# Optimization experiments

Hardware: AMD Instinct MI355X
Metric: run time of the kernel (lower is better)

## Reference

```python
import jax, jax.numpy as jnp
import numpy as np

H = 16
NEG = -1e10

def setup_inputs() -> dict:
    key = jax.random.key(0)
    ks = jax.random.split(key, 12)
    B, S, D = 2, 2048, 1024
    sc = 1.0 / np.sqrt(D)
    inp = {
        'q': jax.random.normal(ks[0], (B, S, D), jnp.float32),
        'k': jax.random.normal(ks[1], (B, S, D), jnp.float32),
        'v': jax.random.normal(ks[2], (B, S, D), jnp.float32),
        'Wq': jax.random.normal(ks[3], (D, D), jnp.float32) * sc,
        'bq': jax.random.normal(ks[4], (D,), jnp.float32) * 0.02,
        'Wk': jax.random.normal(ks[5], (D, D), jnp.float32) * sc,
        'bk': jax.random.normal(ks[6], (D,), jnp.float32) * 0.02,
        'Wv': jax.random.normal(ks[7], (D, D), jnp.float32) * sc,
        'bv': jax.random.normal(ks[8], (D,), jnp.float32) * 0.02,
        'Wo': jax.random.normal(ks[9], (D, D), jnp.float32) * sc,
        'bo': jax.random.normal(ks[10], (D,), jnp.float32) * 0.02,
        'mask': jax.random.randint(ks[11], (B, S, S), 0, 2, jnp.int32),
    }
    return inp

def reference(q, k, v, Wq, bq, Wk, bk, Wv, bv, Wo, bo, mask):
    B, S, D = q.shape
    dk = D // H
    # projections (torch Linear: x @ W.T + b), split heads -> [B,H,S,dk]
    qh = (q @ Wq.T + bq).reshape(B, S, H, dk).transpose(0, 2, 1, 3)
    kh = (k @ Wk.T + bk).reshape(B, S, H, dk).transpose(0, 2, 1, 3)
    vh = (v @ Wv.T + bv).reshape(B, S, H, dk).transpose(0, 2, 1, 3)
    # scaled dot-product scores [B,H,Sq,Sk]
    scores = jnp.einsum('bhqd,bhkd->bhqk', qh, kh) / jnp.sqrt(jnp.float32(dk))
    scores = jnp.where(mask[:, None, :, :] == 0, jnp.float32(NEG), scores)
    attn = jax.nn.softmax(scores, axis=-1)  # dropout in eval mode = identity
    ctx = jnp.einsum('bhqk,bhkd->bhqd', attn, vh)
    concat = ctx.transpose(0, 2, 1, 3).reshape(B, S, D)
    return concat @ Wo.T + bo
```

## Files before the change

### kernel.cpp

```cpp
#include <hip/hip_runtime.h>
#include <hip/hip_bf16.h>
#include <stdint.h>

typedef __bf16 bf16;
typedef __bf16 bf16x2 __attribute__((ext_vector_type(2)));
typedef __bf16 bf16x4 __attribute__((ext_vector_type(4)));
typedef __bf16 bf16x8 __attribute__((ext_vector_type(8)));
typedef float f32x4 __attribute__((ext_vector_type(4)));
typedef float f32x16 __attribute__((ext_vector_type(16)));
typedef unsigned int u32;
typedef u32 u32x4 __attribute__((ext_vector_type(4)));
typedef unsigned long long u64;

#define MFMA16(a, b, c) __builtin_amdgcn_mfma_f32_16x16x32_bf16((a), (b), (c), 0, 0, 0)
#define MFMA32(a, b, c) __builtin_amdgcn_mfma_f32_32x32x16_bf16((a), (b), (c), 0, 0, 0)

constexpr int Bc = 2, Sc = 2048, Dc = 1024, Hc = 16, DKc = 64;
constexpr int Mc = Bc * Sc;
constexpr int MW = Sc / 64;
#define QSCALE 0.1803368801111731f

__device__ __forceinline__ u32 pk2(float a, float b) {
  bf16x2 t; t[0] = (bf16)a; t[1] = (bf16)b;
  return __builtin_bit_cast(u32, t);
}

__device__ __forceinline__ void gl_lds16(const void* g, void* l) {
  __builtin_amdgcn_global_load_lds((const __attribute__((address_space(1))) void*)g,
                                   (__attribute__((address_space(3))) void*)l, 16, 0, 0);
}

__global__ __launch_bounds__(256) void convert_kernel(
    const float* __restrict__ wq, const float* __restrict__ wk,
    const float* __restrict__ wv, const float* __restrict__ wo,
    const float* __restrict__ q, const float* __restrict__ k, const float* __restrict__ v,
    bf16* __restrict__ dwq, bf16* __restrict__ dwk, bf16* __restrict__ dwv,
    bf16* __restrict__ dwo, bf16* __restrict__ dq, bf16* __restrict__ dk,
    bf16* __restrict__ dv) {
  const int y = blockIdx.y;
  const float* src; bf16* dst; size_t n;
  switch (y) {
    case 0: src = wq; dst = dwq; n = (size_t)Dc * Dc; break;
    case 1: src = wk; dst = dwk; n = (size_t)Dc * Dc; break;
    case 2: src = wv; dst = dwv; n = (size_t)Dc * Dc; break;
    case 3: src = wo; dst = dwo; n = (size_t)Dc * Dc; break;
    case 4: src = q;  dst = dq;  n = (size_t)Mc * Dc; break;
    case 5: src = k;  dst = dk;  n = (size_t)Mc * Dc; break;
    default: src = v; dst = dv;  n = (size_t)Mc * Dc; break;
  }
  const size_t i = ((size_t)blockIdx.x * 256 + threadIdx.x) * 8;
  if (i >= n) return;
  const float sc = (y == 0) ? QSCALE : 1.0f;
  f32x4 x0 = *(const f32x4*)&src[i];
  f32x4 x1 = *(const f32x4*)&src[i + 4];
  bf16x8 o;
#pragma unroll
  for (int j = 0; j < 4; ++j) { o[j] = (bf16)(x0[j] * sc); o[4 + j] = (bf16)(x1[j] * sc); }
  *(bf16x8*)&dst[i] = o;
}

__global__ __launch_bounds__(256) void packmask_kernel(const int* __restrict__ mask,
                                                       u64* __restrict__ mbT, int nwords) {
  const int lane = threadIdx.x & 63;
  const int wid = (blockIdx.x * blockDim.x + threadIdx.x) >> 6;
  const int nw = (gridDim.x * blockDim.x) >> 6;
  for (int i = wid; i < nwords; i += nw) {
    int v = mask[(size_t)i * 64 + lane];
    u64 bits = __ballot(v != 0);
    if (lane == 0) {
      const int kw = i & (MW - 1), bq = i >> 5;
      const int b = bq >> 11, q = bq & (Sc - 1);
      mbT[((size_t)(b * MW + kw)) * Sc + q] = bits;
    }
  }
}

__global__ __launch_bounds__(256, 3) void gemm_qkv_kernel(
    const bf16* __restrict__ qb, const bf16* __restrict__ kb, const bf16* __restrict__ vb,
    const bf16* __restrict__ wq, const bf16* __restrict__ wk, const bf16* __restrict__ wv,
    const float* __restrict__ bq, const float* __restrict__ bk, const float* __restrict__ bv,
    bf16* __restrict__ qh, bf16* __restrict__ kh, bf16* __restrict__ vt) {
  __shared__ bf16 As[128 * 64];
  __shared__ bf16 Bs[128 * 64];
  const int d = blockIdx.x;
  const int xcd = d & 7, idx = d >> 3;
  const int proj = idx >> 5, w = idx & 31;
  const int n0 = (w & 7) * 128;
  const int m0 = (xcd * 4 + (w >> 3)) * 128;
  const bf16* Af = proj == 0 ? qb : proj == 1 ? kb : vb;
  const bf16* Bw = proj == 0 ? wq : proj == 1 ? wk : wv;
  const float* bias = proj == 0 ? bq : proj == 1 ? bk : bv;

  const int t = threadIdx.x, lane = t & 63, wv4 = t >> 6;
  const int c = lane & 15, g = lane >> 4;
  const int wr = wv4 >> 1, wc = wv4 & 1;

  f32x4 acc[4][4];
#pragma unroll
  for (int i = 0; i < 4; ++i)
#pragma unroll
    for (int j = 0; j < 4; ++j) acc[i][j] = (f32x4){0.f, 0.f, 0.f, 0.f};

  const int brow_l = lane >> 3;
  const int bslot_l = (lane & 7) ^ brow_l;

  for (int k0 = 0; k0 < Dc; k0 += 64) {
#pragma unroll
    for (int u = 0; u < 4; ++u) {
      const int ch = wv4 * 4 + u;
      const int row = ch * 8 + brow_l;
      gl_lds16(&Af[(size_t)(m0 + row) * Dc + k0 + bslot_l * 8], &As[ch * 512]);
    }
#pragma unroll
    for (int u = 0; u < 4; ++u) {
      const int ch = wv4 * 4 + u;
      const int row = ch * 8 + brow_l;
      gl_lds16(&Bw[(size_t)(n0 + row) * Dc + k0 + bslot_l * 8], &Bs[ch * 512]);
    }
    __syncthreads();
#pragma unroll
    for (int ks = 0; ks < 2; ++ks) {
      bf16x8 af[4], bfr[4];
#pragma unroll
      for (int mt = 0; mt < 4; ++mt) {
        const int row = wr * 64 + mt * 16 + c;
        const int sl = (4 * ks + g) ^ (c & 7);
        af[mt] = *(const bf16x8*)&As[row * 64 + sl * 8];
      }
#pragma unroll
      for (int nt = 0; nt < 4; ++nt) {
        const int row = wc * 64 + nt * 16 + c;
        const int sl = (4 * ks + g) ^ (c & 7);
        bfr[nt] = *(const bf16x8*)&Bs[row * 64 + sl * 8];
      }
#pragma unroll
      for (int mt = 0; mt < 4; ++mt)
#pragma unroll
        for (int nt = 0; nt < 4; ++nt) acc[mt][nt] = MFMA16(af[mt], bfr[nt], acc[mt][nt]);
    }
    __syncthreads();
  }

  const float bsc = proj == 0 ? QSCALE : 1.0f;
  const int colb = n0 + wc * 64 + c;
  const int mrowb = m0 + wr * 64 + 4 * g;
#pragma unroll
  for (int mt = 0; mt < 4; ++mt) {
#pragma unroll
    for (int nt = 0; nt < 4; ++nt) {
      const int col = colb + nt * 16;
      const int mrow = mrowb + mt * 16;
      const float bb = bias[col] * bsc;
      f32x4 a = acc[mt][nt];
      if (proj == 0) {
#pragma unroll
        for (int r = 0; r < 4; ++r) qh[(size_t)(mrow + r) * Dc + col] = (bf16)(a[r] + bb);
      } else if (proj == 1) {
        const int hh = col >> 6, dd = col & 63;
#pragma unroll
        for (int r = 0; r < 4; ++r) {
          const int mr = mrow + r;
          kh[((size_t)((mr >> 11) * Hc + hh) * Sc + (mr & (Sc - 1))) * DKc + dd] = (bf16)(a[r] + bb);
        }
      } else {
        const int batch = mrow >> 11, s = mrow & (Sc - 1);
        const int s2 = (s & ~15) | ((s & 4) << 1) | ((s & 8) >> 1);
        const int hh = col >> 6, dd = col & 63;
        bf16x4 pkv;
#pragma unroll
        for (int r = 0; r < 4; ++r) pkv[r] = (bf16)(a[r] + bb);
        *(bf16x4*)&vt[((size_t)((batch * Hc + hh) * DKc + dd)) * Sc + s2] = pkv;
      }
    }
  }
}

__global__ __launch_bounds__(256, 2) void gemm_o_kernel(const bf16* __restrict__ ctxp,
                                                        const bf16* __restrict__ wo,
                                                        const float* __restrict__ bo,
                                                        float* __restrict__ outp) {
  __shared__ bf16 As[128 * 64];
  __shared__ bf16 Bs[64 * 64];
  const int d = blockIdx.x;
  const int xcd = d & 7, idx = d >> 3;
  const int n0 = (idx & 15) * 64;
  const int m0 = (xcd * 4 + (idx >> 4)) * 128;

  const int t = threadIdx.x, lane = t & 63, wv4 = t >> 6;
  const int c = lane & 15, g = lane >> 4;
  const int brow_l = lane >> 3;
  const int bslot_l = (lane & 7) ^ brow_l;

  f32x4 acc[2][4];
#pragma unroll
  for (int i = 0; i < 2; ++i)
#pragma unroll
    for (int j = 0; j < 4; ++j) acc[i][j] = (f32x4){0.f, 0.f, 0.f, 0.f};

  for (int k0 = 0; k0 < Dc; k0 += 64) {
#pragma unroll
    for (int u = 0; u < 4; ++u) {
      const int ch = wv4 * 4 + u;
      const int row = ch * 8 + brow_l;
      gl_lds16(&ctxp[(size_t)(m0 + row) * Dc + k0 + bslot_l * 8], &As[ch * 512]);
    }
    {
      const int ch = wv4;
      const int row = ch * 8 + brow_l;
      gl_lds16(&wo[(size_t)(n0 + row) * Dc + k0 + bslot_l * 8], &Bs[ch * 512]);
      const int ch2 = 4 + wv4;
      const int row2 = ch2 * 8 + brow_l;
      gl_lds16(&wo[(size_t)(n0 + row2) * Dc + k0 + bslot_l * 8], &Bs[ch2 * 512]);
    }
    __syncthreads();
#pragma unroll
    for (int ks = 0; ks < 2; ++ks) {
      bf16x8 af[2], bfr[4];
#pragma unroll
      for (int mt = 0; mt < 2; ++mt) {
        const int row = wv4 * 32 + mt * 16 + c;
        const int sl = (4 * ks + g) ^ (c & 7);
        af[mt] = *(const bf16x8*)&As[row * 64 + sl * 8];
      }
#pragma unroll
      for (int nt = 0; nt < 4; ++nt) {
        const int row = nt * 16 + c;
        const int sl = (4 * ks + g) ^ (c & 7);
        bfr[nt] = *(const bf16x8*)&Bs[row * 64 + sl * 8];
      }
#pragma unroll
      for (int mt = 0; mt < 2; ++mt)
#pragma unroll
        for (int nt = 0; nt < 4; ++nt) acc[mt][nt] = MFMA16(af[mt], bfr[nt], acc[mt][nt]);
    }
    __syncthreads();
  }

  const int colb = n0 + c;
  const int mrowb = m0 + wv4 * 32 + 4 * g;
#pragma unroll
  for (int mt = 0; mt < 2; ++mt)
#pragma unroll
    for (int nt = 0; nt < 4; ++nt) {
      const int col = colb + nt * 16;
      const int mrow = mrowb + mt * 16;
      const float bb = bo[col];
      f32x4 a = acc[mt][nt];
#pragma unroll
      for (int r = 0; r < 4; ++r) outp[(size_t)(mrow + r) * Dc + col] = a[r] + bb;
    }
}

template <int SPLITS>
__global__ __launch_bounds__(256, 4) void attn_kernel(const bf16* __restrict__ qh,
                                                      const bf16* __restrict__ kh,
                                                      const bf16* __restrict__ vt,
                                                      const u64* __restrict__ mbT,
                                                      bf16* __restrict__ ctx,
                                                      float* __restrict__ opart,
                                                      float2* __restrict__ ml) {
  __shared__ bf16 Ks[2][64 * 64];
  __shared__ bf16 Vs[2][64 * 64];
  const int d = blockIdx.x;
  const int xcd = d & 7, idx = d >> 3;
  int bh, qt, half;
  if constexpr (SPLITS == 2) {
    bh = xcd * 4 + (idx >> 5);
    const int sub = idx & 31;
    qt = sub >> 1; half = sub & 1;
  } else {
    bh = xcd * 4 + (idx >> 4);
    qt = idx & 15; half = 0;
  }
  const int b = bh >> 4, h = bh & 15;
  const int lane = threadIdx.x & 63, wv4 = threadIdx.x >> 6;
  const int ql = lane & 31, hi = lane >> 5;
  const int qrow = qt * 128 + wv4 * 32 + ql;

  const bf16* Qp = qh + (size_t)(b * Sc + qrow) * Dc + h * DKc;
  const bf16* Kp = kh + (size_t)(b * Hc + h) * Sc * DKc;
  const bf16* Vp = vt + (size_t)(b * Hc + h) * DKc * Sc;
  const u64* mbp = mbT + (size_t)b * MW * Sc;

  const int k0 = half * (Sc / SPLITS);
  constexpr int NIT = (Sc / SPLITS) / 64;

  const int srow = lane >> 3, sslot = lane & 7;
  auto stage = [&](int buf, int kt) {
#pragma unroll
    for (int u = 0; u < 2; ++u) {
      const int ch = wv4 * 2 + u;
      const int r = ch * 8 + srow;
      gl_lds16(&Kp[(size_t)(kt + r) * DKc + (size_t)((sslot ^ (r & 7)) * 8)], &Ks[buf][ch * 512]);
    }
#pragma unroll
    for (int u = 0; u < 2; ++u) {
      const int ch = wv4 * 2 + u;
      const int r = ch * 8 + srow;
      gl_lds16(&Vp[(size_t)r * Sc + kt + (size_t)((sslot ^ (r & 7)) * 8)], &Vs[buf][ch * 512]);
    }
  };

  bf16x8 qf[4];
#pragma unroll
  for (int ka = 0; ka < 4; ++ka) qf[ka] = *(const bf16x8*)&Qp[16 * ka + 8 * hi];

  bf16x8 ones8;
#pragma unroll
  for (int j = 0; j < 8; ++j) ones8[j] = (bf16)1.0f;

  f32x16 oacc[2], lacc;
#pragma unroll
  for (int i = 0; i < 2; ++i)
#pragma unroll
    for (int r = 0; r < 16; ++r) oacc[i][r] = 0.f;
#pragma unroll
  for (int r = 0; r < 16; ++r) lacc[r] = 0.f;

  stage(0, k0);
  u64 w = mbp[(size_t)(k0 >> 6) * Sc + qrow];
  asm volatile("s_waitcnt vmcnt(0)" ::: "memory");
  __builtin_amdgcn_s_barrier();
  __builtin_amdgcn_sched_barrier(0);

  for (int it = 0; it < NIT; ++it) {
    const int kt = k0 + it * 64;
    const int buf = it & 1;
    const int ktn = (it + 1 < NIT) ? kt + 64 : kt;
    stage(buf ^ 1, ktn);
    const u64 wn = mbp[(size_t)(ktn >> 6) * Sc + qrow];

    f32x16 st[2];
#pragma unroll
    for (int tt = 0; tt < 2; ++tt) {
      const int row = 32 * tt + ql;
      const bf16* kbase = &Ks[buf][row * 64];
      f32x16 z;
#pragma unroll
      for (int r = 0; r < 16; ++r) z[r] = 0.f;
      __builtin_amdgcn_s_setprio(1);
#pragma unroll
      for (int ka = 0; ka < 4; ++ka) {
        bf16x8 kf = *(const bf16x8*)&kbase[((2 * ka + hi) ^ (row & 7)) * 8];
        z = MFMA32(kf, qf[ka], z);
      }
      __builtin_amdgcn_s_setprio(0);
      st[tt] = z;
    }

    const u32 wt0 = (u32)(w >> (4 * hi));
    const u32 wt1 = (u32)(w >> (32 + 4 * hi));
#pragma unroll
    for (int tt = 0; tt < 2; ++tt) {
      const u32 wt = tt ? wt1 : wt0;
#pragma unroll
      for (int r = 0; r < 16; ++r) {
        const int bit = (r & 3) + 8 * (r >> 2);
        const float p = __builtin_amdgcn_exp2f((float)st[tt][r]);
        st[tt][r] = ((wt >> bit) & 1u) ? p : 0.f;
      }
    }

    u32x4 pb[4];
#pragma unroll
    for (int ks = 0; ks < 4; ++ks) {
      const int tt = ks >> 1, e = ks & 1;
#pragma unroll
      for (int w2 = 0; w2 < 4; ++w2)
        pb[ks][w2] = pk2((float)st[tt][8 * e + 2 * w2], (float)st[tt][8 * e + 2 * w2 + 1]);
    }

    __builtin_amdgcn_s_setprio(1);
#pragma unroll
    for (int ks = 0; ks < 4; ++ks)
      lacc = MFMA32(ones8, __builtin_bit_cast(bf16x8, pb[ks]), lacc);
#pragma unroll
    for (int dt = 0; dt < 2; ++dt) {
      const int row = 32 * dt + ql;
      const bf16* vbase = &Vs[buf][row * 64];
#pragma unroll
      for (int ks = 0; ks < 4; ++ks) {
        bf16x8 vf = *(const bf16x8*)&vbase[((2 * ks + hi) ^ (row & 7)) * 8];
        oacc[dt] = MFMA32(vf, __builtin_bit_cast(bf16x8, pb[ks]), oacc[dt]);
      }
    }
    __builtin_amdgcn_s_setprio(0);

    asm volatile("s_waitcnt vmcnt(0)" ::: "memory");
    __builtin_amdgcn_s_barrier();
    __builtin_amdgcn_sched_barrier(0);
    w = wn;
  }

  const float lsum = lacc[0];
  if constexpr (SPLITS == 2) {
    float* opr = opart + ((size_t)(half * 32 + bh) * Sc + qrow) * 64;
#pragma unroll
    for (int dt = 0; dt < 2; ++dt)
#pragma unroll
      for (int i = 0; i < 4; ++i) {
        f32x4 o4;
#pragma unroll
        for (int rr = 0; rr < 4; ++rr) o4[rr] = oacc[dt][4 * i + rr];
        *(f32x4*)&opr[32 * dt + 8 * i + 4 * hi] = o4;
      }
    if (hi == 0) {
      float2 v2; v2.x = 0.f; v2.y = lsum;
      ml[(size_t)(half * 32 + bh) * Sc + qrow] = v2;
    }
  } else {
    const float rinv = 1.f / fmaxf(lsum, 1e-35f);
    bf16* cp = ctx + (size_t)(b * Sc + qrow) * Dc + h * DKc;
#pragma unroll
    for (int dt = 0; dt < 2; ++dt)
#pragma unroll
      for (int i = 0; i < 4; ++i) {
        bf16x4 o4;
#pragma unroll
        for (int rr = 0; rr < 4; ++rr) o4[rr] = (bf16)(oacc[dt][4 * i + rr] * rinv);
        *(bf16x4*)&cp[32 * dt + 8 * i + 4 * hi] = o4;
      }
  }
}

__global__ __launch_bounds__(256) void combine_kernel(const float* __restrict__ op,
                                                      const float2* __restrict__ ml,
                                                      bf16* __restrict__ ctx) {
  const int wv = threadIdx.x >> 6, lane = threadIdx.x & 63;
  const size_t row = (size_t)blockIdx.x * 4 + wv;
  const int bh = (int)(row >> 11), q = (int)(row & 2047);
  const int b = bh >> 4, h = bh & 15;
  const float2 ml0 = ml[row], ml1 = ml[65536 + row];
  const float o0 = op[row * 64 + lane];
  const float o1 = op[(size_t)65536 * 64 + row * 64 + lane];
  const float m = fmaxf(ml0.x, ml1.x);
  const float a0 = exp2f(ml0.x - m), a1 = exp2f(ml1.x - m);
  const float l = fmaxf(a0 * ml0.y + a1 * ml1.y, 1e-35f);
  const float o = (a0 * o0 + a1 * o1) / l;
  ctx[((size_t)(b * Sc + q)) * Dc + h * DKc + lane] = (bf16)o;
}

extern "C" void kernel_launch(void* const* d_in, const int* in_sizes, int n_in,
                              void* d_out, int out_size, void* d_ws, size_t ws_size,
                              hipStream_t stream) {
  (void)in_sizes; (void)n_in; (void)out_size;
  const float* q  = (const float*)d_in[0];
  const float* k  = (const float*)d_in[1];
  const float* v  = (const float*)d_in[2];
  const float* Wq = (const float*)d_in[3];
  const float* bq = (const float*)d_in[4];
  const float* Wk = (const float*)d_in[5];
  const float* bk = (const float*)d_in[6];
  const float* Wv = (const float*)d_in[7];
  const float* bv = (const float*)d_in[8];
  const float* Wo = (const float*)d_in[9];
  const float* bo = (const float*)d_in[10];
  const int* mask = (const int*)d_in[11];

  char* ws = (char*)d_ws;
  size_t off = 0;
  auto take = [&](size_t bytes) -> void* {
    void* p = ws + off;
    off += (bytes + 255) & ~(size_t)255;
    return p;
  };
  bf16* qh  = (bf16*)take((size_t)Mc * Dc * 2);
  bf16* kh  = (bf16*)take((size_t)Mc * Dc * 2);
  bf16* vt  = (bf16*)take((size_t)Mc * Dc * 2);
  bf16* ctx = (bf16*)take((size_t)Mc * Dc * 2);
  u64* mbits = (u64*)take((size_t)Bc * Sc * MW * 8);
  bf16* wqb = (bf16*)take((size_t)Dc * Dc * 2);
  bf16* wkb = (bf16*)take((size_t)Dc * Dc * 2);
  bf16* wvb = (bf16*)take((size_t)Dc * Dc * 2);
  bf16* wob = (bf16*)take((size_t)Dc * Dc * 2);
  bf16* qb  = (bf16*)take((size_t)Mc * Dc * 2);
  bf16* kb  = (bf16*)take((size_t)Mc * Dc * 2);
  bf16* vb  = (bf16*)take((size_t)Mc * Dc * 2);
  float* opart = (float*)take((size_t)2 * 32 * Sc * 64 * 4);
  float2* mlb = (float2*)take((size_t)2 * 32 * Sc * 8);
  const bool split2 = off <= ws_size;

  convert_kernel<<<dim3(2048, 7), 256, 0, stream>>>(Wq, Wk, Wv, Wo, q, k, v,
                                                    wqb, wkb, wvb, wob, qb, kb, vb);
  packmask_kernel<<<512, 256, 0, stream>>>(mask, mbits, Bc * Sc * Sc / 64);
  gemm_qkv_kernel<<<768, 256, 0, stream>>>(qb, kb, vb, wqb, wkb, wvb, bq, bk, bv, qh, kh, vt);
  if (split2) {
    attn_kernel<2><<<1024, 256, 0, stream>>>(qh, kh, vt, mbits, ctx, opart, mlb);
    combine_kernel<<<16384, 256, 0, stream>>>(opart, mlb, ctx);
  } else {
    attn_kernel<1><<<512, 256, 0, stream>>>(qh, kh, vt, mbits, ctx, opart, mlb);
  }
  gemm_o_kernel<<<512, 256, 0, stream>>>(ctx, wob, bo, (float*)d_out);
}
```

Measured before the change: 170.4 us.

## Split attention KV range four ways, fuse mask packing into convert kernel

Adds a 4-way split-K attention path (2048 blocks) with a templated combine that sums partial outputs and row sums, and simplifies the combine by dropping the unused max term. The attention kernel is now allowed 5 waves per SIMD in its launch bounds, and the mask bit-packing is folded into the conversion kernel as an extra grid row, removing one launch. The aim is more parallelism and occupancy in attention plus less launch overhead. The cost is more partial-result traffic through the combine step and tighter register limits.

```diff
diff --git a/kernel.cpp b/kernel.cpp
--- a/kernel.cpp
+++ b/kernel.cpp
@@ -30,14 +30,31 @@
                                    (__attribute__((address_space(3))) void*)l, 16, 0, 0);
 }
 
-__global__ __launch_bounds__(256) void convert_kernel(
+__global__ __launch_bounds__(256) void prep_kernel(
     const float* __restrict__ wq, const float* __restrict__ wk,
     const float* __restrict__ wv, const float* __restrict__ wo,
     const float* __restrict__ q, const float* __restrict__ k, const float* __restrict__ v,
+    const int* __restrict__ mask,
     bf16* __restrict__ dwq, bf16* __restrict__ dwk, bf16* __restrict__ dwv,
     bf16* __restrict__ dwo, bf16* __restrict__ dq, bf16* __restrict__ dk,
-    bf16* __restrict__ dv) {
+    bf16* __restrict__ dv, u64* __restrict__ mbT) {
   const int y = blockIdx.y;
+  if (y == 7) {
+    const int lane = threadIdx.x & 63;
+    const int wid = (blockIdx.x * blockDim.x + threadIdx.x) >> 6;
+    const int nw = (gridDim.x * blockDim.x) >> 6;
+    const int nwords = Bc * Sc * Sc / 64;
+    for (int i = wid; i < nwords; i += nw) {
+      int vv = mask[(size_t)i * 64 + lane];
+      u64 bits = __ballot(vv != 0);
+      if (lane == 0) {
+        const int kw = i & (MW - 1), bq = i >> 5;
+        const int b = bq >> 11, qq = bq & (Sc - 1);
+        mbT[((size_t)(b * MW + kw)) * Sc + qq] = bits;
+      }
+    }
+    return;
+  }
   const float* src; bf16* dst; size_t n;
   switch (y) {
     case 0: src = wq; dst = dwq; n = (size_t)Dc * Dc; break;
@@ -57,22 +74,6 @@
 #pragma unroll
   for (int j = 0; j < 4; ++j) { o[j] = (bf16)(x0[j] * sc); o[4 + j] = (bf16)(x1[j] * sc); }
   *(bf16x8*)&dst[i] = o;
-}
-
-__global__ __launch_bounds__(256) void packmask_kernel(const int* __restrict__ mask,
-                                                       u64* __restrict__ mbT, int nwords) {
-  const int lane = threadIdx.x & 63;
-  const int wid = (blockIdx.x * blockDim.x + threadIdx.x) >> 6;
-  const int nw = (gridDim.x * blockDim.x) >> 6;
-  for (int i = wid; i < nwords; i += nw) {
-    int v = mask[(size_t)i * 64 + lane];
-    u64 bits = __ballot(v != 0);
-    if (lane == 0) {
-      const int kw = i & (MW - 1), bq = i >> 5;
-      const int b = bq >> 11, q = bq & (Sc - 1);
-      mbT[((size_t)(b * MW + kw)) * Sc + q] = bits;
-    }
-  }
 }
 
 __global__ __launch_bounds__(256, 3) void gemm_qkv_kernel(
@@ -252,26 +253,20 @@
 }
 
 template <int SPLITS>
-__global__ __launch_bounds__(256, 4) void attn_kernel(const bf16* __restrict__ qh,
+__global__ __launch_bounds__(256, 5) void attn_kernel(const bf16* __restrict__ qh,
                                                       const bf16* __restrict__ kh,
                                                       const bf16* __restrict__ vt,
                                                       const u64* __restrict__ mbT,
                                                       bf16* __restrict__ ctx,
                                                       float* __restrict__ opart,
-                                                      float2* __restrict__ ml) {
+                                                      float* __restrict__ lsums) {
   __shared__ bf16 Ks[2][64 * 64];
   __shared__ bf16 Vs[2][64 * 64];
   const int d = blockIdx.x;
   const int xcd = d & 7, idx = d >> 3;
-  int bh, qt, half;
-  if constexpr (SPLITS == 2) {
-    bh = xcd * 4 + (idx >> 5);
-    const int sub = idx & 31;
-    qt = sub >> 1; half = sub & 1;
-  } else {
-    bh = xcd * 4 + (idx >> 4);
-    qt = idx & 15; half = 0;
-  }
+  const int bh = xcd * 4 + idx / (16 * SPLITS);
+  const int sub = idx % (16 * SPLITS);
+  const int qt = sub / SPLITS, half = sub % SPLITS;
   const int b = bh >> 4, h = bh & 15;
   const int lane = threadIdx.x & 63, wv4 = threadIdx.x >> 6;
   const int ql = lane & 31, hi = lane >> 5;
@@ -393,7 +388,7 @@
   }
 
   const float lsum = lacc[0];
-  if constexpr (SPLITS == 2) {
+  if constexpr (SPLITS > 1) {
     float* opr = opart + ((size_t)(half * 32 + bh) * Sc + qrow) * 64;
 #pragma unroll
     for (int dt = 0; dt < 2; ++dt)
@@ -404,10 +399,7 @@
         for (int rr = 0; rr < 4; ++rr) o4[rr] = oacc[dt][4 * i + rr];
         *(f32x4*)&opr[32 * dt + 8 * i + 4 * hi] = o4;
       }
-    if (hi == 0) {
-      float2 v2; v2.x = 0.f; v2.y = lsum;
-      ml[(size_t)(half * 32 + bh) * Sc + qrow] = v2;
-    }
+    if (hi == 0) lsums[(size_t)(half * 32 + bh) * Sc + qrow] = lsum;
   } else {
     const float rinv = 1.f / fmaxf(lsum, 1e-35f);
     bf16* cp = ctx + (size_t)(b * Sc + qrow) * Dc + h * DKc;
@@ -423,21 +415,21 @@
   }
 }
 
+template <int NS>
 __global__ __launch_bounds__(256) void combine_kernel(const float* __restrict__ op,
-                                                      const float2* __restrict__ ml,
+                                                      const float* __restrict__ ls,
                                                       bf16* __restrict__ ctx) {
   const int wv = threadIdx.x >> 6, lane = threadIdx.x & 63;
   const size_t row = (size_t)blockIdx.x * 4 + wv;
   const int bh = (int)(row >> 11), q = (int)(row & 2047);
   const int b = bh >> 4, h = bh & 15;
-  const float2 ml0 = ml[row], ml1 = ml[65536 + row];
-  const float o0 = op[row * 64 + lane];
-  const float o1 = op[(size_t)65536 * 64 + row * 64 + lane];
-  const float m = fmaxf(ml0.x, ml1.x);
-  const float a0 = exp2f(ml0.x - m), a1 = exp2f(ml1.x - m);
-  const float l = fmaxf(a0 * ml0.y + a1 * ml1.y, 1e-35f);
-  const float o = (a0 * o0 + a1 * o1) / l;
-  ctx[((size_t)(b * Sc + q)) * Dc + h * DKc + lane] = (bf16)o;
+  float o = 0.f, l = 0.f;
+#pragma unroll
+  for (int s = 0; s < NS; ++s) {
+    o += op[(size_t)s * 65536 * 64 + row * 64 + lane];
+    l += ls[(size_t)s * 65536 + row];
+  }
+  ctx[((size_t)(b * Sc + q)) * Dc + h * DKc + lane] = (bf16)(o / fmaxf(l, 1e-35f));
 }
 
 extern "C" void kernel_launch(void* const* d_in, const int* in_sizes, int n_in,
@@ -476,19 +468,31 @@
   bf16* qb  = (bf16*)take((size_t)Mc * Dc * 2);
   bf16* kb  = (bf16*)take((size_t)Mc * Dc * 2);
   bf16* vb  = (bf16*)take((size_t)Mc * Dc * 2);
-  float* opart = (float*)take((size_t)2 * 32 * Sc * 64 * 4);
-  float2* mlb = (float2*)take((size_t)2 * 32 * Sc * 8);
-  const bool split2 = off <= ws_size;
-
-  convert_kernel<<<dim3(2048, 7), 256, 0, stream>>>(Wq, Wk, Wv, Wo, q, k, v,
-                                                    wqb, wkb, wvb, wob, qb, kb, vb);
-  packmask_kernel<<<512, 256, 0, stream>>>(mask, mbits, Bc * Sc * Sc / 64);
+
+  const size_t opart_sz = (size_t)32 * Sc * 64 * 4;
+  const size_t ls_sz    = (size_t)32 * Sc * 4;
+  int splits = 1;
+  float* opart = nullptr; float* lsums = nullptr;
+  for (int s = 4; s >= 2; s >>= 1) {
+    if (off + (opart_sz + ls_sz) * s <= ws_size) {
+      splits = s;
+      opart = (float*)(ws + off);
+      lsums = (float*)(ws + off + opart_sz * s);
+      break;
+    }
+  }
+
+  prep_kernel<<<dim3(2048, 8), 256, 0, stream>>>(Wq, Wk, Wv, Wo, q, k, v, mask,
+                                                 wqb, wkb, wvb, wob, qb, kb, vb, mbits);
   gemm_qkv_kernel<<<768, 256, 0, stream>>>(qb, kb, vb, wqb, wkb, wvb, bq, bk, bv, qh, kh, vt);
-  if (split2) {
-    attn_kernel<2><<<1024, 256, 0, stream>>>(qh, kh, vt, mbits, ctx, opart, mlb);
-    combine_kernel<<<16384, 256, 0, stream>>>(opart, mlb, ctx);
+  if (splits == 4) {
+    attn_kernel<4><<<2048, 256, 0, stream>>>(qh, kh, vt, mbits, ctx, opart, lsums);
+    combine_kernel<4><<<16384, 256, 0, stream>>>(opart, lsums, ctx);
+  } else if (splits == 2) {
+    attn_kernel<2><<<1024, 256, 0, stream>>>(qh, kh, vt, mbits, ctx, opart, lsums);
+    combine_kernel<2><<<16384, 256, 0, stream>>>(opart, lsums, ctx);
   } else {
-    attn_kernel<1><<<512, 256, 0, stream>>>(qh, kh, vt, mbits, ctx, opart, mlb);
+    attn_kernel<1><<<512, 256, 0, stream>>>(qh, kh, vt, mbits, ctx, opart, lsums);
   }
   gemm_o_kernel<<<512, 256, 0, stream>>>(ctx, wob, bo, (float*)d_out);
 }
```

Measured after the change: 312.6 us. 83.4% more time.
